# Kernel tuning notes

Measured on AMD Instinct MI355X. Metric: run time of the kernel, lower is better.

## Reference

```python
import jax, jax.numpy as jnp
import numpy as np

PATCH = 768
POS = 64
HID = 512
B, N = 8, 2048


def setup_inputs() -> dict:
    key = jax.random.key(0)
    ks = jax.random.split(key, 8)
    d_in = PATCH + POS
    s = 1.0 / np.sqrt(d_in)
    return {
        "patches": jax.random.normal(ks[0], (B, N, PATCH), jnp.float32),
        "positions": jax.random.normal(ks[1], (B, N, POS), jnp.float32),
        "Wq": jax.random.uniform(ks[2], (d_in, HID), jnp.float32, -s, s),
        "bq": jax.random.uniform(ks[3], (HID,), jnp.float32, -s, s),
        "Wk": jax.random.uniform(ks[4], (d_in, HID), jnp.float32, -s, s),
        "bk": jax.random.uniform(ks[5], (d_in and HID,), jnp.float32, -s, s),
        "Wv": jax.random.uniform(ks[6], (d_in, HID), jnp.float32, -s, s),
        "bv": jax.random.uniform(ks[7], (HID,), jnp.float32, -s, s),
    }


def reference(patches, positions, Wq, bq, Wk, bk, Wv, bv):
    # concat patch features with positional features: [B, N, PATCH+POS]
    x = jnp.concatenate([patches, positions], axis=-1)
    Q = x @ Wq + bq  # [B, N, HID]
    K = x @ Wk + bk
    V = x @ Wv + bv
    scale = jnp.sqrt(jnp.asarray(HID, x.dtype))
    scores = jnp.einsum("bnd,bmd->bnm", Q, K) / scale  # [B, N, N]
    weights = jax.nn.softmax(scores, axis=-1)
    return jnp.einsum("bnm,bmd->bnd", weights, V)  # [B, N, HID]
```

## Files before the change

### kernel.cpp

```cpp
#include <hip/hip_runtime.h>
#include <hip/hip_bf16.h>
#include <math.h>

typedef __hip_bfloat16 bf16;
typedef __attribute__((ext_vector_type(4))) float f32x4;
typedef __attribute__((ext_vector_type(8))) short s16x8;

typedef const __attribute__((address_space(1))) void gvoid_t;
typedef __attribute__((address_space(3))) void lvoid_t;

__device__ __forceinline__ void gload16(const void* g, void* l) {
  __builtin_amdgcn_global_load_lds((gvoid_t*)g, (lvoid_t*)l, 16, 0, 0);
}
__device__ __forceinline__ unsigned short f2b(float f) {
  bf16 h = __float2bfloat16(f);
  return *(unsigned short*)&h;
}

__global__ __launch_bounds__(256) void prep_x(const float* __restrict__ patches,
                                              const float* __restrict__ positions,
                                              bf16* __restrict__ xb) {
  const long long row = blockIdx.x;
  const int c = threadIdx.x;
  const bool lo = (c < 192);
  const bool hi = (c >= 192) && (c < 208);
  const float* src = lo ? (patches + row * 768 + c * 4)
                        : (positions + row * 64 + (c - 192) * 4);
  if (lo || hi) {
    float4 v = *(const float4*)src;
    const int dst = lo ? (c * 4) : (768 + (c - 192) * 4);
    uint2 w;
    w.x = (unsigned int)f2b(v.x) | ((unsigned int)f2b(v.y) << 16);
    w.y = (unsigned int)f2b(v.z) | ((unsigned int)f2b(v.w) << 16);
    *(uint2*)(xb + row * 832 + dst) = w;
  }
}

__global__ __launch_bounds__(256) void prep_w(const float* __restrict__ Wq,
                                              const float* __restrict__ Wk,
                                              const float* __restrict__ Wv,
                                              bf16* __restrict__ Wt) {
  __shared__ float tile[32][33];
  const int z = blockIdx.z;
  const float* W = (z == 0) ? Wq : (z == 1) ? Wk : Wv;
  bf16* T = Wt + (long long)z * 512 * 832;
  const int n0 = blockIdx.x * 32;
  const int k0 = blockIdx.y * 32;
  const int tx = threadIdx.x, ty = threadIdx.y;
  #pragma unroll
  for (int i = 0; i < 32; i += 8)
    tile[ty + i][tx] = W[(long long)(k0 + ty + i) * 512 + n0 + tx];
  __syncthreads();
  #pragma unroll
  for (int i = 0; i < 32; i += 8)
    T[(long long)(n0 + ty + i) * 832 + k0 + tx] = __float2bfloat16(tile[tx][ty + i]);
}

#define VMW8 asm volatile("s_waitcnt vmcnt(8)" ::: "memory")
#define PBAR do { __builtin_amdgcn_s_barrier(); __builtin_amdgcn_sched_barrier(0); } while (0)

__device__ __forceinline__ void stage_half(const bf16* src, char* lds, int stride) {
  gload16(src, lds);
  gload16(src + 64 * stride, lds + 8192);
}
__device__ __forceinline__ void lda4(const bf16* base, int rowbase, int llo,
                                     int xk0, int xk1, s16x8 af[4][2]) {
  #pragma unroll
  for (int mf = 0; mf < 4; mf++) {
    const bf16* p = base + (rowbase + mf * 16 + llo) * 64;
    af[mf][0] = *(const s16x8*)(p + xk0);
    af[mf][1] = *(const s16x8*)(p + xk1);
  }
}
__device__ __forceinline__ void ldb2(const bf16* base, int rowbase, int llo,
                                     int xk0, int xk1, s16x8 bfr[2][2]) {
  #pragma unroll
  for (int nf = 0; nf < 2; nf++) {
    const bf16* p = base + (rowbase + nf * 16 + llo) * 64;
    bfr[nf][0] = *(const s16x8*)(p + xk0);
    bfr[nf][1] = *(const s16x8*)(p + xk1);
  }
}
__device__ __forceinline__ void mma16(f32x4 acc[4][2], s16x8 af[4][2],
                                      s16x8 bfr[2][2]) {
  __builtin_amdgcn_s_setprio(1);
  #pragma unroll
  for (int mf = 0; mf < 4; mf++)
    #pragma unroll
    for (int nf = 0; nf < 2; nf++) {
      acc[mf][nf] = __builtin_amdgcn_mfma_f32_16x16x32_bf16(
          af[mf][0], bfr[nf][0], acc[mf][nf], 0, 0, 0);
      acc[mf][nf] = __builtin_amdgcn_mfma_f32_16x16x32_bf16(
          af[mf][1], bfr[nf][1], acc[mf][nf], 0, 0, 0);
    }
  __builtin_amdgcn_s_setprio(0);
}

__global__ __launch_bounds__(512, 2) void gemm_qkv(
    const bf16* __restrict__ xb, const bf16* __restrict__ Wt,
    const float* __restrict__ bq, const float* __restrict__ bk,
    const float* __restrict__ bv,
    bf16* __restrict__ qk, bf16* __restrict__ vt) {
  __shared__ bf16 As[2][256 * 64];
  __shared__ bf16 Bs[2][256 * 64];
  const int tid = threadIdx.x;
  const int wave = tid >> 6, lane = tid & 63;
  const int llo = lane & 15, lhi = lane >> 4;
  const int wm = wave >> 2, wn = wave & 3;

  const unsigned int lin = blockIdx.x;
  const unsigned int xcd = lin & 7u, idx = lin >> 3;
  const unsigned int g = xcd * 48u + idx;
  const unsigned int bm_t = g / 6u;
  const unsigned int bn_t = g - bm_t * 6u;
  const int row0 = (int)bm_t * 256;
  const int col0 = (int)bn_t * 256;
  const int z = col0 >> 9;

  const int sr = tid >> 3;
  const int kkofs = ((tid & 7) ^ (sr & 7)) << 3;
  const bf16* sA = xb + (long long)(row0 + sr) * 832 + kkofs;
  const bf16* sB = Wt + (long long)(col0 + sr) * 832 + kkofs;
  const int wofs = wave * 1024;

  const int xk0 = ((lhi ^ (llo & 7)) << 3);
  const int xk1 = (((4 + lhi) ^ (llo & 7)) << 3);

  f32x4 acc[2][2][4][2] = {};
  s16x8 af[4][2], bf0[2][2], bf1[2][2];

  stage_half(sA, (char*)As[0] + wofs, 832);
  stage_half(sB, (char*)Bs[0] + wofs, 832);
  stage_half(sB + 128 * 832, (char*)Bs[0] + 16384 + wofs, 832);
  stage_half(sA + 128 * 832, (char*)As[0] + 16384 + wofs, 832);
  stage_half(sA + 64, (char*)As[1] + wofs, 832);
  stage_half(sB + 64, (char*)Bs[1] + wofs, 832);
  VMW8; PBAR;

  for (int i = 0; i < 6; ++i) {
    const int kt1 = (2 * i + 1) * 64;
    const int kt2 = (2 * i + 2 <= 12) ? (2 * i + 2) * 64 : 768;
    const int kt3 = (2 * i + 3 <= 12) ? (2 * i + 3) * 64 : 768;
    lda4(As[0], wm * 64, llo, xk0, xk1, af);
    ldb2(Bs[0], wn * 32, llo, xk0, xk1, bf0);
    stage_half(sB + 128 * 832 + kt1, (char*)Bs[1] + 16384 + wofs, 832);
    VMW8; PBAR;
    mma16(acc[0][0], af, bf0);
    ldb2(Bs[0], 128 + wn * 32, llo, xk0, xk1, bf1);
    stage_half(sA + 128 * 832 + kt1, (char*)As[1] + 16384 + wofs, 832);
    VMW8; PBAR;
    mma16(acc[0][1], af, bf1);
    lda4(As[0], 128 + wm * 64, llo, xk0, xk1, af);
    stage_half(sA + kt2, (char*)As[0] + wofs, 832);
    PBAR;
    mma16(acc[1][0], af, bf0);
    stage_half(sB + kt2, (char*)Bs[0] + wofs, 832);
    VMW8; PBAR;
    mma16(acc[1][1], af, bf1);
    lda4(As[1], wm * 64, llo, xk0, xk1, af);
    ldb2(Bs[1], wn * 32, llo, xk0, xk1, bf0);
    stage_half(sB + 128 * 832 + kt2, (char*)Bs[0] + 16384 + wofs, 832);
    VMW8; PBAR;
    mma16(acc[0][0], af, bf0);
    ldb2(Bs[1], 128 + wn * 32, llo, xk0, xk1, bf1);
    stage_half(sA + 128 * 832 + kt2, (char*)As[0] + 16384 + wofs, 832);
    VMW8; PBAR;
    mma16(acc[0][1], af, bf1);
    lda4(As[1], 128 + wm * 64, llo, xk0, xk1, af);
    stage_half(sA + kt3, (char*)As[1] + wofs, 832);
    PBAR;
    mma16(acc[1][0], af, bf0);
    stage_half(sB + kt3, (char*)Bs[1] + wofs, 832);
    VMW8; PBAR;
    mma16(acc[1][1], af, bf1);
  }

  asm volatile("s_waitcnt vmcnt(4)" ::: "memory");
  PBAR;
  lda4(As[0], wm * 64, llo, xk0, xk1, af);
  ldb2(Bs[0], wn * 32, llo, xk0, xk1, bf0);
  ldb2(Bs[0], 128 + wn * 32, llo, xk0, xk1, bf1);
  mma16(acc[0][0], af, bf0);
  mma16(acc[0][1], af, bf1);
  lda4(As[0], 128 + wm * 64, llo, xk0, xk1, af);
  mma16(acc[1][0], af, bf0);
  mma16(acc[1][1], af, bf1);

  if (z < 2) {
    const float* bias = z ? bk : bq;
    bf16* outp = qk + (long long)z * 16384 * 512;
    #pragma unroll
    for (int qr = 0; qr < 2; qr++)
      #pragma unroll
      for (int qc = 0; qc < 2; qc++)
        #pragma unroll
        for (int mf = 0; mf < 4; mf++)
          #pragma unroll
          for (int nf = 0; nf < 2; nf++) {
            const int c = (col0 & 511) + qc * 128 + wn * 32 + nf * 16 + llo;
            const int grow0 = row0 + qr * 128 + wm * 64 + mf * 16 + lhi * 4;
            const float bb = bias[c];
            #pragma unroll
            for (int r = 0; r < 4; r++)
              outp[(long long)(grow0 + r) * 512 + c] =
                  __float2bfloat16(acc[qr][qc][mf][nf][r] + bb);
          }
  } else {
    #pragma unroll
    for (int qr = 0; qr < 2; qr++)
      #pragma unroll
      for (int qc = 0; qc < 2; qc++)
        #pragma unroll
        for (int mf = 0; mf < 4; mf++)
          #pragma unroll
          for (int nf = 0; nf < 2; nf++) {
            const int c = (col0 & 511) + qc * 128 + wn * 32 + nf * 16 + llo;
            const int grow0 = row0 + qr * 128 + wm * 64 + mf * 16 + lhi * 4;
            const int b = grow0 >> 11, j = grow0 & 2047;
            const float bb = bv[c];
            uint2 w;
            w.x = (unsigned int)f2b(acc[qr][qc][mf][nf][0] + bb) |
                  ((unsigned int)f2b(acc[qr][qc][mf][nf][1] + bb) << 16);
            w.y = (unsigned int)f2b(acc[qr][qc][mf][nf][2] + bb) |
                  ((unsigned int)f2b(acc[qr][qc][mf][nf][3] + bb) << 16);
            *(uint2*)(vt + (long long)b * 512 * 2048 + (long long)c * 2048 + j) = w;
          }
  }
}

__global__ __launch_bounds__(512, 2) void gemm_scores(const bf16* __restrict__ qk,
                                                      bf16* __restrict__ S,
                                                      float* __restrict__ rowsumP) {
  __shared__ bf16 As[2][256 * 64];
  __shared__ bf16 Bs[2][256 * 64];
  const int tid = threadIdx.x;
  const int wave = tid >> 6, lane = tid & 63;
  const int llo = lane & 15, lhi = lane >> 4;
  const int wm = wave >> 2, wn = wave & 3;

  const unsigned int lin = blockIdx.x;
  const int b = (int)(lin & 7u);
  const unsigned int idx = lin >> 3;
  const int row0 = (int)(idx >> 3) * 256;
  const int coltile = (int)(idx & 7u);
  const int col0 = coltile * 256;

  const bf16* Ab = qk + (long long)b * 2048 * 512;
  const bf16* Bb = qk + (long long)16384 * 512 + (long long)b * 2048 * 512;

  const int sr = tid >> 3;
  const int kkofs = ((tid & 7) ^ (sr & 7)) << 3;
  const bf16* sA = Ab + (long long)(row0 + sr) * 512 + kkofs;
  const bf16* sB = Bb + (long long)(col0 + sr) * 512 + kkofs;
  const int wofs = wave * 1024;

  const int xk0 = ((lhi ^ (llo & 7)) << 3);
  const int xk1 = (((4 + lhi) ^ (llo & 7)) << 3);

  f32x4 acc[2][2][4][2] = {};
  s16x8 af[4][2], bf0[2][2], bf1[2][2];

  stage_half(sA, (char*)As[0] + wofs, 512);
  stage_half(sB, (char*)Bs[0] + wofs, 512);
  stage_half(sB + 128 * 512, (char*)Bs[0] + 16384 + wofs, 512);
  stage_half(sA + 128 * 512, (char*)As[0] + 16384 + wofs, 512);
  stage_half(sA + 64, (char*)As[1] + wofs, 512);
  stage_half(sB + 64, (char*)Bs[1] + wofs, 512);
  VMW8; PBAR;

  for (int i = 0; i < 4; ++i) {
    const int kt1 = (2 * i + 1) * 64;
    const int kt2 = (2 * i + 2 < 8) ? (2 * i + 2) * 64 : 448;
    const int kt3 = (2 * i + 3 < 8) ? (2 * i + 3) * 64 : 448;
    lda4(As[0], wm * 64, llo, xk0, xk1, af);
    ldb2(Bs[0], wn * 32, llo, xk0, xk1, bf0);
    stage_half(sB + 128 * 512 + kt1, (char*)Bs[1] + 16384 + wofs, 512);
    VMW8; PBAR;
    mma16(acc[0][0], af, bf0);
    ldb2(Bs[0], 128 + wn * 32, llo, xk0, xk1, bf1);
    stage_half(sA + 128 * 512 + kt1, (char*)As[1] + 16384 + wofs, 512);
    VMW8; PBAR;
    mma16(acc[0][1], af, bf1);
    lda4(As[0], 128 + wm * 64, llo, xk0, xk1, af);
    stage_half(sA + kt2, (char*)As[0] + wofs, 512);
    PBAR;
    mma16(acc[1][0], af, bf0);
    stage_half(sB + kt2, (char*)Bs[0] + wofs, 512);
    VMW8; PBAR;
    mma16(acc[1][1], af, bf1);
    lda4(As[1], wm * 64, llo, xk0, xk1, af);
    ldb2(Bs[1], wn * 32, llo, xk0, xk1, bf0);
    stage_half(sB + 128 * 512 + kt2, (char*)Bs[0] + 16384 + wofs, 512);
    VMW8; PBAR;
    mma16(acc[0][0], af, bf0);
    ldb2(Bs[1], 128 + wn * 32, llo, xk0, xk1, bf1);
    stage_half(sA + 128 * 512 + kt2, (char*)As[0] + 16384 + wofs, 512);
    VMW8; PBAR;
    mma16(acc[0][1], af, bf1);
    lda4(As[1], 128 + wm * 64, llo, xk0, xk1, af);
    stage_half(sA + kt3, (char*)As[1] + wofs, 512);
    PBAR;
    mma16(acc[1][0], af, bf0);
    stage_half(sB + kt3, (char*)Bs[1] + wofs, 512);
    VMW8; PBAR;
    mma16(acc[1][1], af, bf1);
  }

  __syncthreads();

  const float alpha = 0.044194173824159216f;
  bf16* Sb = S + (long long)b * 2048 * 2048;
  #pragma unroll
  for (int qr = 0; qr < 2; qr++)
    #pragma unroll
    for (int qc = 0; qc < 2; qc++)
      #pragma unroll
      for (int mf = 0; mf < 4; mf++)
        #pragma unroll
        for (int nf = 0; nf < 2; nf++) {
          #pragma unroll
          for (int r = 0; r < 4; r++)
            acc[qr][qc][mf][nf][r] = __expf(acc[qr][qc][mf][nf][r] * alpha);
          const int gcol = col0 + qc * 128 + wn * 32 + nf * 16 + llo;
          const int grow0 = row0 + qr * 128 + wm * 64 + mf * 16 + lhi * 4;
          #pragma unroll
          for (int r = 0; r < 4; r++)
            Sb[(long long)(grow0 + r) * 2048 + gcol] =
                __float2bfloat16(acc[qr][qc][mf][nf][r]);
        }

  float* psum = (float*)As;
  #pragma unroll
  for (int qr = 0; qr < 2; qr++)
    #pragma unroll
    for (int mf = 0; mf < 4; mf++)
      #pragma unroll
      for (int r = 0; r < 4; r++) {
        float p = acc[qr][0][mf][0][r] + acc[qr][0][mf][1][r] +
                  acc[qr][1][mf][0][r] + acc[qr][1][mf][1][r];
        p += __shfl_xor(p, 1, 64);
        p += __shfl_xor(p, 2, 64);
        p += __shfl_xor(p, 4, 64);
        p += __shfl_xor(p, 8, 64);
        if (llo == 0)
          psum[wn * 256 + qr * 128 + wm * 64 + mf * 16 + lhi * 4 + r] = p;
      }
  __syncthreads();
  if (tid < 256) {
    const float v = psum[tid] + psum[256 + tid] + psum[512 + tid] + psum[768 + tid];
    rowsumP[(long long)(b * 8 + coltile) * 2048 + row0 + tid] = v;
  }
}

__global__ __launch_bounds__(256) void reduce_rowsum(
    const float* __restrict__ rowsumP, float* __restrict__ rinv) {
  const int i = blockIdx.x * 256 + threadIdx.x;
  const int b = i >> 11, row = i & 2047;
  const float* p = rowsumP + ((long long)b * 8) * 2048 + row;
  float s = 0.f;
  #pragma unroll
  for (int t = 0; t < 8; t++) s += p[t * 2048];
  rinv[i] = 1.0f / s;
}

__global__ __launch_bounds__(256) void gemm_pv(const bf16* __restrict__ S,
                                               const bf16* __restrict__ vt,
                                               const float* __restrict__ rinv,
                                               float* __restrict__ out) {
  __shared__ bf16 As[128 * 64];
  __shared__ bf16 Bs[128 * 64];
  const int tid = threadIdx.x;
  const int wave = tid >> 6, lane = tid & 63;
  const int llo = lane & 15, lhi = lane >> 4;
  const int wm = wave >> 1, wn = wave & 1;

  const unsigned int lin = blockIdx.x;
  const unsigned int xcd = lin & 7u, idx = lin >> 3;
  const int b = (int)xcd;
  const int row0 = (int)(idx >> 2) * 128;
  const int col0 = (int)(idx & 3u) * 128;

  const bf16* Ab = S + (long long)b * 2048 * 2048;
  const bf16* Bb = vt + (long long)b * 512 * 2048;

  f32x4 acc[4][4] = {};
  for (int kt = 0; kt < 2048; kt += 64) {
    #pragma unroll
    for (int i = 0; i < 4; i++) {
      const int c = i * 256 + tid;
      const int r = c >> 3, cc = c & 7;
      const int kk = (cc ^ (r & 7)) << 3;
      gload16(Ab + ((long long)(row0 + r) * 2048 + kt + kk),
              (char*)As + (long long)(i * 256 + wave * 64) * 16);
      gload16(Bb + ((long long)(col0 + r) * 2048 + kt + kk),
              (char*)Bs + (long long)(i * 256 + wave * 64) * 16);
    }
    __syncthreads();
    #pragma unroll
    for (int k0 = 0; k0 < 64; k0 += 32) {
      const int xk = ((((k0 >> 3) + lhi) ^ (llo & 7)) << 3);
      s16x8 af[4], bfr[4];
      #pragma unroll
      for (int mf = 0; mf < 4; mf++)
        af[mf] = *(const s16x8*)&As[(wm * 64 + mf * 16 + llo) * 64 + xk];
      #pragma unroll
      for (int nf = 0; nf < 4; nf++)
        bfr[nf] = *(const s16x8*)&Bs[(wn * 64 + nf * 16 + llo) * 64 + xk];
      #pragma unroll
      for (int mf = 0; mf < 4; mf++)
        #pragma unroll
        for (int nf = 0; nf < 4; nf++)
          acc[mf][nf] = __builtin_amdgcn_mfma_f32_16x16x32_bf16(
              af[mf], bfr[nf], acc[mf][nf], 0, 0, 0);
    }
    __syncthreads();
  }

  const float* rs = rinv + (long long)b * 2048;
  float* Ob = out + (long long)b * 2048 * 512;
  #pragma unroll
  for (int mf = 0; mf < 4; mf++) {
    const int grow0 = row0 + wm * 64 + mf * 16 + lhi * 4;
    float iv[4];
    #pragma unroll
    for (int r = 0; r < 4; r++) iv[r] = rs[grow0 + r];
    #pragma unroll
    for (int nf = 0; nf < 4; nf++) {
      const int gcol = col0 + wn * 64 + nf * 16 + llo;
      #pragma unroll
      for (int r = 0; r < 4; r++)
        Ob[(long long)(grow0 + r) * 512 + gcol] = acc[mf][nf][r] * iv[r];
    }
  }
}

extern "C" void kernel_launch(void* const* d_in, const int* in_sizes, int n_in,
                              void* d_out, int out_size, void* d_ws, size_t ws_size,
                              hipStream_t stream) {
  const float* patches = (const float*)d_in[0];
  const float* positions = (const float*)d_in[1];
  const float* Wq = (const float*)d_in[2];
  const float* bq = (const float*)d_in[3];
  const float* Wk = (const float*)d_in[4];
  const float* bk = (const float*)d_in[5];
  const float* Wv = (const float*)d_in[6];
  const float* bv = (const float*)d_in[7];
  float* out = (float*)d_out;

  if (ws_size < 149422080u) return;

  char* ws = (char*)d_ws;
  bf16* Wt = (bf16*)(ws);
  bf16* xb = (bf16*)(ws + 2555904);
  bf16* qk = (bf16*)(ws + 29818880);
  bf16* vt = (bf16*)(ws + 63373312);
  bf16* S  = (bf16*)(ws + 80150528);
  float* rinv    = (float*)(ws + 147259392);
  float* rowsumP = (float*)(ws + 147324928);

  prep_x<<<16384, 256, 0, stream>>>(patches, positions, xb);
  prep_w<<<dim3(16, 26, 3), dim3(32, 8), 0, stream>>>(Wq, Wk, Wv, Wt);
  gemm_qkv<<<384, 512, 0, stream>>>(xb, Wt, bq, bk, bv, qk, vt);
  gemm_scores<<<512, 512, 0, stream>>>(qk, S, rowsumP);
  reduce_rowsum<<<64, 256, 0, stream>>>(rowsumP, rinv);
  gemm_pv<<<512, 256, 0, stream>>>(S, vt, rinv, out);
}
```

Baseline: 261.6 us.

## Rewrite PV GEMM with 256x128 tiles and triple-buffered async LDS pipeline

The PV GEMM moves from a 128x128 tile with 256 threads and a synchronous load/compute loop to a 256x128 tile with 512 threads. It now uses a three-stage LDS ring fed by direct global-to-LDS loads, with vmcnt waits and barriers that overlap loading the next k-slice with MFMA work on the current one. The larger tile halves the grid and improves reuse of the V tile. A vmcnt(0) drain is also added before the QKV epilogue. The cost is higher LDS use per block (about 144 KB) and a fragile hand-tuned wait schedule.

```diff
diff --git a/kernel.cpp b/kernel.cpp
--- a/kernel.cpp
+++ b/kernel.cpp
@@ -56,7 +56,8 @@
     T[(long long)(n0 + ty + i) * 832 + k0 + tx] = __float2bfloat16(tile[tx][ty + i]);
 }
 
-#define VMW8 asm volatile("s_waitcnt vmcnt(8)" ::: "memory")
+#define VMW8  asm volatile("s_waitcnt vmcnt(8)" ::: "memory")
+#define VMW10 asm volatile("s_waitcnt vmcnt(10)" ::: "memory")
 #define PBAR do { __builtin_amdgcn_s_barrier(); __builtin_amdgcn_sched_barrier(0); } while (0)
 
 __device__ __forceinline__ void stage_half(const bf16* src, char* lds, int stride) {
@@ -185,6 +186,7 @@
   lda4(As[0], 128 + wm * 64, llo, xk0, xk1, af);
   mma16(acc[1][0], af, bf0);
   mma16(acc[1][1], af, bf1);
+  asm volatile("s_waitcnt vmcnt(0)" ::: "memory");
 
   if (z < 2) {
     const float* bias = z ? bk : bq;
@@ -363,76 +365,94 @@
   rinv[i] = 1.0f / s;
 }
 
-__global__ __launch_bounds__(256) void gemm_pv(const bf16* __restrict__ S,
-                                               const bf16* __restrict__ vt,
-                                               const float* __restrict__ rinv,
-                                               float* __restrict__ out) {
-  __shared__ bf16 As[128 * 64];
-  __shared__ bf16 Bs[128 * 64];
+#define PV_TILE(c, cs, kstage)                                              \
+  do {                                                                      \
+                                                              \
+    lda4(As3[c], wm * 64, llo, xk0, xk1, af);                               \
+    ldb2(Bs3[c], wn * 32, llo, xk0, xk1, bfr);                              \
+    stage_half(sA + (kstage), (char*)As3[cs] + wofs, 2048);                 \
+    stage_half(sB + (kstage), (char*)Bs3[cs] + wofs, 2048);                 \
+    VMW10; PBAR;                                                            \
+    mma16(acc[0], af, bfr);                                                 \
+                              \
+    lda4(As3[c], 128 + wm * 64, llo, xk0, xk1, af);                         \
+    stage_half(sA + 128 * 2048 + (kstage), (char*)As3[cs] + 16384 + wofs,   \
+               2048);                                                       \
+    VMW8; PBAR;                                                             \
+    mma16(acc[1], af, bfr);                                                 \
+  } while (0)
+
+__global__ __launch_bounds__(512, 2) void gemm_pv(const bf16* __restrict__ S,
+                                                  const bf16* __restrict__ vt,
+                                                  const float* __restrict__ rinv,
+                                                  float* __restrict__ out) {
+  __shared__ bf16 As3[3][256 * 64];
+  __shared__ bf16 Bs3[3][128 * 64];
   const int tid = threadIdx.x;
   const int wave = tid >> 6, lane = tid & 63;
   const int llo = lane & 15, lhi = lane >> 4;
-  const int wm = wave >> 1, wn = wave & 1;
+  const int wm = wave >> 2, wn = wave & 3;
 
   const unsigned int lin = blockIdx.x;
-  const unsigned int xcd = lin & 7u, idx = lin >> 3;
-  const int b = (int)xcd;
-  const int row0 = (int)(idx >> 2) * 128;
+  const int b = (int)(lin & 7u);
+  const unsigned int idx = lin >> 3;
+  const int row0 = (int)(idx >> 2) * 256;
   const int col0 = (int)(idx & 3u) * 128;
 
   const bf16* Ab = S + (long long)b * 2048 * 2048;
   const bf16* Bb = vt + (long long)b * 512 * 2048;
 
-  f32x4 acc[4][4] = {};
-  for (int kt = 0; kt < 2048; kt += 64) {
-    #pragma unroll
-    for (int i = 0; i < 4; i++) {
-      const int c = i * 256 + tid;
-      const int r = c >> 3, cc = c & 7;
-      const int kk = (cc ^ (r & 7)) << 3;
-      gload16(Ab + ((long long)(row0 + r) * 2048 + kt + kk),
-              (char*)As + (long long)(i * 256 + wave * 64) * 16);
-      gload16(Bb + ((long long)(col0 + r) * 2048 + kt + kk),
-              (char*)Bs + (long long)(i * 256 + wave * 64) * 16);
-    }
-    __syncthreads();
-    #pragma unroll
-    for (int k0 = 0; k0 < 64; k0 += 32) {
-      const int xk = ((((k0 >> 3) + lhi) ^ (llo & 7)) << 3);
-      s16x8 af[4], bfr[4];
-      #pragma unroll
-      for (int mf = 0; mf < 4; mf++)
-        af[mf] = *(const s16x8*)&As[(wm * 64 + mf * 16 + llo) * 64 + xk];
-      #pragma unroll
-      for (int nf = 0; nf < 4; nf++)
-        bfr[nf] = *(const s16x8*)&Bs[(wn * 64 + nf * 16 + llo) * 64 + xk];
-      #pragma unroll
-      for (int mf = 0; mf < 4; mf++)
-        #pragma unroll
-        for (int nf = 0; nf < 4; nf++)
-          acc[mf][nf] = __builtin_amdgcn_mfma_f32_16x16x32_bf16(
-              af[mf], bfr[nf], acc[mf][nf], 0, 0, 0);
-    }
-    __syncthreads();
-  }
+  const int sr = tid >> 3;
+  const int kkofs = ((tid & 7) ^ (sr & 7)) << 3;
+  const bf16* sA = Ab + (long long)(row0 + sr) * 2048 + kkofs;
+  const bf16* sB = Bb + (long long)(col0 + sr) * 2048 + kkofs;
+  const int wofs = wave * 1024;
+
+  const int xk0 = ((lhi ^ (llo & 7)) << 3);
+  const int xk1 = (((4 + lhi) ^ (llo & 7)) << 3);
+
+  f32x4 acc[2][4][2] = {};
+  s16x8 af[4][2], bfr[2][2];
+
+  stage_half(sA, (char*)As3[0] + wofs, 2048);
+  stage_half(sB, (char*)Bs3[0] + wofs, 2048);
+  stage_half(sA + 128 * 2048, (char*)As3[0] + 16384 + wofs, 2048);
+  stage_half(sA + 64, (char*)As3[1] + wofs, 2048);
+  stage_half(sB + 64, (char*)Bs3[1] + wofs, 2048);
+  stage_half(sA + 128 * 2048 + 64, (char*)As3[1] + 16384 + wofs, 2048);
+  VMW8; PBAR;
+
+  for (int j = 0; j < 10; ++j) {
+    const int kb = j * 192;
+    PV_TILE(0, 2, kb + 128);
+    PV_TILE(1, 0, kb + 192);
+    PV_TILE(2, 1, kb + 256);
+  }
+  PV_TILE(0, 2, 1984);
+  PV_TILE(1, 0, 1984);
+
+  asm volatile("s_waitcnt vmcnt(0)" ::: "memory");
 
   const float* rs = rinv + (long long)b * 2048;
   float* Ob = out + (long long)b * 2048 * 512;
   #pragma unroll
-  for (int mf = 0; mf < 4; mf++) {
-    const int grow0 = row0 + wm * 64 + mf * 16 + lhi * 4;
-    float iv[4];
-    #pragma unroll
-    for (int r = 0; r < 4; r++) iv[r] = rs[grow0 + r];
-    #pragma unroll
-    for (int nf = 0; nf < 4; nf++) {
-      const int gcol = col0 + wn * 64 + nf * 16 + llo;
-      #pragma unroll
-      for (int r = 0; r < 4; r++)
-        Ob[(long long)(grow0 + r) * 512 + gcol] = acc[mf][nf][r] * iv[r];
+  for (int qr = 0; qr < 2; qr++)
+    #pragma unroll
+    for (int mf = 0; mf < 4; mf++) {
+      const int grow0 = row0 + qr * 128 + wm * 64 + mf * 16 + lhi * 4;
+      float iv[4];
+      #pragma unroll
+      for (int r = 0; r < 4; r++) iv[r] = rs[grow0 + r];
+      #pragma unroll
+      for (int nf = 0; nf < 2; nf++) {
+        const int gcol = col0 + wn * 32 + nf * 16 + llo;
+        #pragma unroll
+        for (int r = 0; r < 4; r++)
+          Ob[(long long)(grow0 + r) * 512 + gcol] = acc[qr][mf][nf][r] * iv[r];
+      }
     }
-  }
-}
+}
+#undef PV_TILE
 
 extern "C" void kernel_launch(void* const* d_in, const int* in_sizes, int n_in,
                               void* d_out, int out_size, void* d_ws, size_t ws_size,
@@ -463,5 +483,5 @@
   gemm_qkv<<<384, 512, 0, stream>>>(xb, Wt, bq, bk, bv, qk, vt);
   gemm_scores<<<512, 512, 0, stream>>>(qk, S, rowsumP);
   reduce_rowsum<<<64, 256, 0, stream>>>(rowsumP, rinv);
-  gemm_pv<<<512, 256, 0, stream>>>(S, vt, rinv, out);
-}
+  gemm_pv<<<256, 512, 0, stream>>>(S, vt, rinv, out);
+}
```

Result: no change. 264.0 us (+0.9%).
